# Performance work log

Hardware: AMD Instinct MI355X
Metric: run time of the kernel (lower is better)

The kernel has to match this reference:

```python
import jax, jax.numpy as jnp
import numpy as np

K = 3          # stencil half-width
SIGMA = 0.05   # shock proximity length scale
DX = 0.02      # spatial step
HID = 64       # flux net hidden dim
IN_FEAT = (2 * K + 1) * 3 + 1  # 22


def setup_inputs() -> dict:
    key = jax.random.key(0)
    ks = jax.random.split(key, 10)
    B, nt, nx = 16, 64, 1024
    grid_input = jax.random.uniform(ks[0], (B, 1, nt, nx), jnp.float32)
    dt = jax.random.uniform(ks[1], (B,), jnp.float32) * 0.01  # CFL-like dt
    s = lambda k, sh: jax.random.normal(k, sh, jnp.float32) * 0.1
    return {
        "grid_input": grid_input,
        "dt": dt,
        "W0": s(ks[2], (HID, IN_FEAT)), "b0": s(ks[3], (HID,)),
        "W1": s(ks[4], (HID, HID)),     "b1": s(ks[5], (HID,)),
        "W2": s(ks[6], (HID, HID)),     "b2": s(ks[7], (HID,)),
        "W3": s(ks[8], (1, HID)),       "b3": s(ks[9], (1,)),
    }


def reference(grid_input, dt, W0, b0, W1, b1, W2, b2, W3, b3):
    B, _, nt, nx = grid_input.shape
    k, dx, S = K, DX, 2 * K + 1
    dtype = grid_input.dtype

    # static gather indices for the stencil unfold (into the padded array)
    idx = jnp.arange(nx)[:, None] + jnp.arange(S)[None, :]  # (nx, S)
    # static distance matrix cell-center vs interface (computed once, reused every step)
    cell_centers = (jnp.arange(nx, dtype=dtype) + 0.5) * dx          # (nx,)
    interface_pos = jnp.arange(1, nx, dtype=dtype) * dx              # (nx-1,)
    dist = jnp.abs(cell_centers[:, None] - interface_pos[None, :])   # (nx, nx-1)

    dt3 = dt[:, None, None]  # (B,1,1)

    def unfold(x):  # (B,1,nx) -> (B,S,nx) replicate-padded sliding windows
        p = jnp.pad(x[:, 0, :], ((0, 0), (k, k)), mode="edge")  # (B, nx+2k)
        return jnp.transpose(p[:, idx], (0, 2, 1))              # (B,S,nx)

    def shock_proximity(state):  # (B,1,nx) -> (B,1,nx), detached
        st = jax.lax.stop_gradient(state)
        rL, rR = st[:, 0, :-1], st[:, 0, 1:]
        char_L = 1.0 - 2.0 * rL           # f'(rho) for LWR flux rho(1-rho)
        char_R = 1.0 - 2.0 * rR
        s_rh = 1.0 - rL - rR              # Rankine-Hugoniot shock speed
        is_shock = (char_L > s_rh) & (s_rh > char_R)      # (B, nx-1)
        masked = jnp.where(is_shock[:, None, :], dist[None], jnp.asarray(1e6, dtype))
        min_dist = masked.min(axis=2)                     # (B, nx)
        any_shock = jnp.any(is_shock, axis=1, keepdims=True).astype(dtype)
        return (jnp.exp(-min_dist / SIGMA) * any_shock)[:, None, :]

    gelu = lambda h: jax.nn.gelu(h, approximate=False)

    def flux_net(f):  # (B, IN_FEAT, nx) -> (B, 1, nx); dropout inactive (eval)
        h = jnp.einsum("oc,bcn->bon", W0, f) + b0[None, :, None]
        h = jnp.einsum("oc,bcn->bon", W1, gelu(h)) + b1[None, :, None]
        h = jnp.einsum("oc,bcn->bon", W2, gelu(h)) + b2[None, :, None]
        return jnp.einsum("oc,bcn->bon", W3, gelu(h)) + b3[None, :, None]

    def step(state, _):
        stencil_vals = unfold(state)                      # (B,S,nx)
        char_speeds = 1.0 - 2.0 * stencil_vals            # flux.derivative
        prox = shock_proximity(state)                     # (B,1,nx)
        stencil_prox = unfold(prox)                       # (B,S,nx)
        dt_channel = jnp.broadcast_to(dt3, (B, 1, nx))
        feats = jnp.concatenate([stencil_vals, char_speeds, stencil_prox, dt_channel], axis=1)
        update = flux_net(feats)                          # (B,1,nx)
        new_state = jnp.clip(state + dt3 / dx * update, 0.0, 1.0)
        return new_state, new_state

    state0 = grid_input[:, :, 0, :]                       # (B,1,nx)
    _, ys = jax.lax.scan(step, state0, None, length=nt - 1)  # (nt-1,B,1,nx)
    out = jnp.concatenate([state0[:, :, None, :], jnp.transpose(ys, (1, 2, 0, 3))], axis=2)
    return out  # (B,1,nt,nx)
```

## Files before the change

kernel.cpp:

```cpp
#include <hip/hip_runtime.h>

#define NX 1024
#define NT 64
#define NBATCH 16
#define BPB 64
#define NBLK (NBATCH * BPB)
#define DXC 0.02f
#define INV_SIG 20.0f
#define BIGF 1.0e6f

typedef __attribute__((ext_vector_type(8))) short bf16x8;
typedef __attribute__((ext_vector_type(4))) float f32x4;
typedef unsigned long long u64t;

__device__ __forceinline__ unsigned short f2bf(float x) {
    unsigned u = __builtin_bit_cast(unsigned, x);
    u += 0x7FFFu + ((u >> 16) & 1u);
    return (unsigned short)(u >> 16);
}
__device__ __forceinline__ float bf2f(unsigned short h) {
    return __builtin_bit_cast(float, (unsigned)h << 16);
}
__device__ __forceinline__ unsigned cvt_pk_bf16(float lo, float hi) {
    unsigned r;
    asm("v_cvt_pk_bf16_f32 %0, %1, %2" : "=v"(r) : "v"(lo), "v"(hi));
    return r;
}
__device__ __forceinline__ float hw_exp2(float v) {
    float e;
    asm("v_exp_f32 %0, %1" : "=v"(e) : "v"(v));
    return e;
}

__device__ __forceinline__ float fast_gelu(float x) {
    float x2 = x * x;
    float v  = x * fmaf(0.1029456f, x2, 2.3022654f);
    float rc = __builtin_amdgcn_rcpf(hw_exp2(v) + 1.0f);
    return x - x * rc;
}

__device__ __forceinline__ u64t sys_load_u64(const u64t* p) {
    return __hip_atomic_load(p, __ATOMIC_RELAXED, __HIP_MEMORY_SCOPE_SYSTEM);
}
__device__ __forceinline__ void sys_store_u64(u64t* p, u64t v) {
    __hip_atomic_store(p, v, __ATOMIC_RELAXED, __HIP_MEMORY_SCOPE_SYSTEM);
}

__device__ __forceinline__ int swz(int row, int k) {
    return (row << 6) + ((((k >> 3) ^ row) & 7) << 3) + (k & 7);
}

__global__ void __launch_bounds__(256, 4) nfv_kernel(
    const float* __restrict__ grid, const float* __restrict__ dtp,
    const float* __restrict__ W0, const float* __restrict__ b0,
    const float* __restrict__ W1, const float* __restrict__ b1,
    const float* __restrict__ W2, const float* __restrict__ b2,
    const float* __restrict__ W3, const float* __restrict__ b3,
    float* __restrict__ outp, u64t* __restrict__ halo)
{
    __shared__ float st_s[80];
    __shared__ __align__(16) unsigned short feat_s[16 * 64];
    __shared__ __align__(16) unsigned short actA[16 * 64];
    __shared__ __align__(16) unsigned short actB[16 * 64];
    __shared__ __align__(16) float part_s[16 * 20];

    const int tid  = threadIdx.x;
    const int lane = tid & 63;
    const int wid  = tid >> 6;
    const int bid  = blockIdx.x;
    const int b    = bid >> 6;
    const int bb   = bid & 63;
    const int c0   = bb * 16;
    const float dtv = dtp[b];
    const float r   = dtv / DXC;
    const float b3v = b3[0];

    const float* grow = grid + (size_t)b * (NT * NX);
    float*       orow = outp + (size_t)b * (NT * NX);

    const int l15 = lane & 15;
    const int kb0 = lane >> 4;
    const int col = wid * 16 + l15;
    const int row0 = (lane >> 4) << 2;
    const int arow = l15;

    bf16x8 w0f, w1fa, w1fb, w2fa, w2fb;
    {
        const int k0 = kb0 * 8;
        #pragma unroll
        for (int i = 0; i < 8; ++i) {
            int k = k0 + i;
            float wv;
            if (k < 7)       wv = W0[col * 22 + k] - 2.0f * W0[col * 22 + 7 + k];
            else if (k < 14) wv = W0[col * 22 + (k - 7)] - 2.0f * W0[col * 22 + k];
            else if (k < 22) wv = W0[col * 22 + k];
            else             wv = 0.0f;
            w0f[i]  = (short)f2bf(wv);
            w1fa[i] = (short)f2bf(W1[col * 64 + k0 + i]);
            w1fb[i] = (short)f2bf(W1[col * 64 + k0 + 32 + i]);
            w2fa[i] = (short)f2bf(W2[col * 64 + k0 + i]);
            w2fb[i] = (short)f2bf(W2[col * 64 + k0 + 32 + i]);
        }
    }
    float bias0 = b0[col];
    #pragma unroll
    for (int k = 7; k < 14; ++k) bias0 += W0[col * 22 + k];
    const float bias1 = b1[col], bias2 = b2[col], w3c = W3[col];

    const int aoffA = (arow << 6) + (((kb0    ) ^ arow) * 8 & 56);
    const int aoffB = (arow << 6) + ((((kb0+4) ^ arow) & 7) << 3);
    const bf16x8* const prF  = (const bf16x8*)(const void*)&feat_s[aoffA];
    const bf16x8* const prA0 = (const bf16x8*)(const void*)&actA[aoffA];
    const bf16x8* const prA1 = (const bf16x8*)(const void*)&actA[aoffB];
    const bf16x8* const prB0 = (const bf16x8*)(const void*)&actB[aoffA];
    const bf16x8* const prB1 = (const bf16x8*)(const void*)&actB[aoffB];
    unsigned short* const pwA0 = &actA[swz(row0    , col)];
    unsigned short* const pwA1 = &actA[swz(row0 + 1, col)];
    unsigned short* const pwA2 = &actA[swz(row0 + 2, col)];
    unsigned short* const pwA3 = &actA[swz(row0 + 3, col)];
    unsigned short* const pwB0 = &actB[swz(row0    , col)];
    unsigned short* const pwB1 = &actB[swz(row0 + 1, col)];
    unsigned short* const pwB2 = &actB[swz(row0 + 2, col)];
    unsigned short* const pwB3 = &actB[swz(row0 + 3, col)];
    const int poff = row0 * 20 + (wid << 2) + (l15 >> 2);
    const bool pwrite = ((l15 & 3) == 0);

    const int fslot = wid * 2 + (lane >> 5);
    const int frow  = lane & 15;
    const bool fact = (fslot < 7) && ((lane & 31) < 16);
    int fc = frow + 29 + fslot;
    if (bb == 0       && fc < 32) fc = 32;
    if (bb == BPB - 1 && fc > 47) fc = 47;
    const int foff0 = swz(frow, fslot);
    const int foff1 = swz(frow, 7 + fslot);
    const int foff2 = swz(frow, 14 + fslot);

    int hg = (lane < 32) ? (c0 - 32 + lane) : (c0 - 16 + lane);
    hg = hg < 0 ? 0 : (hg > NX - 1 ? NX - 1 : hg);
    const u64t* const hbase = &halo[(size_t)(b * BPB + (hg >> 4)) * 64 + (hg & 15)];
    const int hdst = (lane < 32) ? lane : lane + 16;

    const f32x4* const pru = (const f32x4*)(const void*)&part_s[l15 * 20];
    u64t* const hpub = &halo[(size_t)bid * 64 + l15];
    float* const ocell = orow + c0 + l15;

    ((unsigned*)feat_s)[tid]       = 0;
    ((unsigned*)feat_s)[tid + 256] = 0;
    if (tid < 16) {
        orow[c0 + tid] = grow[c0 + tid];
        feat_s[swz(tid, 21)] = f2bf(dtv);
    }
    if (tid < 80) {
        int ga = c0 - 32 + tid;
        ga = ga < 0 ? 0 : (ga > NX - 1 ? NX - 1 : ga);
        st_s[tid] = grow[ga];
    }

    for (int t = 1; t < NT; ++t) {
        if (wid == 0 && t >= 2) {
            const unsigned need = (unsigned)(t - 1);
            const u64t* src = hbase + (size_t)(((t - 1) & 3) * 16);
            u64t u;
            do { u = sys_load_u64(src); } while ((unsigned)(u >> 32) < need);
            st_s[hdst] = __builtin_bit_cast(float, (unsigned)u);
        }
        __syncthreads();

        {
            bool q0 = st_s[lane + 1] > st_s[lane];
            bool q1 = (lane < 15) && (st_s[65 + lane] > st_s[64 + lane]);
            u64t m0 = __ballot(q0);
            u64t m1 = __ballot(q1);
            if (fact) {
                const int c = fc;
                float dL = BIGF, dR = BIGF;
                u64t sello = m0 & (((u64t)1 << c) - 1);
                if (sello) dL = (float)(c - (63 - __builtin_clzll(sello))) - 0.5f;
                u64t r0 = m0 >> c;
                if (r0)      dR = (float)__builtin_ctzll(r0) + 0.5f;
                else if (m1) dR = (float)(64 - c + __builtin_ctzll(m1)) + 0.5f;
                float d = fminf(dL, dR);
                float prox = hw_exp2(d * -0.5770780f);

                float sv = st_s[c];
                unsigned short shi = f2bf(sv);
                unsigned short slo = f2bf(sv - bf2f(shi));
                feat_s[foff0] = shi;
                feat_s[foff1] = slo;
                feat_s[foff2] = f2bf(prox);
            }
        }
        __syncthreads();

        {
            f32x4 c4 = {0.0f, 0.0f, 0.0f, 0.0f};
            c4 = __builtin_amdgcn_mfma_f32_16x16x32_bf16(*prF, w0f, c4, 0, 0, 0);
            unsigned u01 = cvt_pk_bf16(fast_gelu(c4[0] + bias0), fast_gelu(c4[1] + bias0));
            unsigned u23 = cvt_pk_bf16(fast_gelu(c4[2] + bias0), fast_gelu(c4[3] + bias0));
            *pwA0 = (unsigned short)u01;
            *pwA1 = (unsigned short)(u01 >> 16);
            *pwA2 = (unsigned short)u23;
            *pwA3 = (unsigned short)(u23 >> 16);
        }
        __syncthreads();

        {
            f32x4 c4 = {0.0f, 0.0f, 0.0f, 0.0f};
            c4 = __builtin_amdgcn_mfma_f32_16x16x32_bf16(*prA0, w1fa, c4, 0, 0, 0);
            c4 = __builtin_amdgcn_mfma_f32_16x16x32_bf16(*prA1, w1fb, c4, 0, 0, 0);
            unsigned u01 = cvt_pk_bf16(fast_gelu(c4[0] + bias1), fast_gelu(c4[1] + bias1));
            unsigned u23 = cvt_pk_bf16(fast_gelu(c4[2] + bias1), fast_gelu(c4[3] + bias1));
            *pwB0 = (unsigned short)u01;
            *pwB1 = (unsigned short)(u01 >> 16);
            *pwB2 = (unsigned short)u23;
            *pwB3 = (unsigned short)(u23 >> 16);
        }
        __syncthreads();

        {
            f32x4 c4 = {0.0f, 0.0f, 0.0f, 0.0f};
            c4 = __builtin_amdgcn_mfma_f32_16x16x32_bf16(*prB0, w2fa, c4, 0, 0, 0);
            c4 = __builtin_amdgcn_mfma_f32_16x16x32_bf16(*prB1, w2fb, c4, 0, 0, 0);
            #pragma unroll
            for (int j = 0; j < 4; ++j) {
                float p = w3c * fast_gelu(c4[j] + bias2);
                p += __shfl_xor(p, 1);
                p += __shfl_xor(p, 2);
                if (pwrite) part_s[poff + j * 20] = p;
            }
        }
        __syncthreads();

        if (wid == 0 && lane < 16) {
            f32x4 s4 = pru[0] + pru[1] + pru[2] + pru[3];
            float sum = s4[0] + s4[1] + s4[2] + s4[3];
            float ns = st_s[32 + l15] + r * (sum + b3v);
            ns = fminf(1.0f, fmaxf(0.0f, ns));
            if (t < NT - 1) {
                u64t u = ((u64t)(unsigned)t << 32) |
                         (u64t)(unsigned)__builtin_bit_cast(unsigned, ns);
                sys_store_u64(hpub + (size_t)((t & 3) * 16), u);
            }
            ocell[(size_t)t * NX] = ns;
            st_s[32 + l15] = ns;
        }
    }
}

extern "C" void kernel_launch(void* const* d_in, const int* in_sizes, int n_in,
                              void* d_out, int out_size, void* d_ws, size_t ws_size,
                              hipStream_t stream) {
    const float* grid = (const float*)d_in[0];
    const float* dtp  = (const float*)d_in[1];
    const float* W0   = (const float*)d_in[2];
    const float* b0   = (const float*)d_in[3];
    const float* W1   = (const float*)d_in[4];
    const float* b1   = (const float*)d_in[5];
    const float* W2   = (const float*)d_in[6];
    const float* b2   = (const float*)d_in[7];
    const float* W3   = (const float*)d_in[8];
    const float* b3   = (const float*)d_in[9];
    float* outp = (float*)d_out;

    u64t* halo = (u64t*)d_ws;

    hipMemsetAsync(d_ws, 0, (size_t)NBLK * 64 * sizeof(u64t), stream);

    void* args[] = {(void*)&grid, (void*)&dtp, (void*)&W0, (void*)&b0,
                    (void*)&W1, (void*)&b1, (void*)&W2, (void*)&b2,
                    (void*)&W3, (void*)&b3, (void*)&outp, (void*)&halo};

    int maxb = 0;
    hipError_t qe = hipOccupancyMaxActiveBlocksPerMultiprocessor(
        &maxb, (const void*)nfv_kernel, 256, 0);
    if (qe == hipSuccess && maxb >= 4) {
        hipLaunchCooperativeKernel((const void*)nfv_kernel,
                                   dim3(NBLK), dim3(256), args, 0, stream);
    } else {
        hipLaunchKernelGGL(nfv_kernel, dim3(NBLK), dim3(256), 0, stream,
                           grid, dtp, W0, b0, W1, b1, W2, b2, W3, b3,
                           outp, halo);
    }
}
```

Before: 188.4 us.

## Collapse each block to a single wavefront and replace barriers with wave fences

Each 256-thread block becomes one 64-lane wavefront that computes all four 16-column output tiles of every MLP layer itself. This lets the per-layer __syncthreads barriers become lgkmcnt waits, and the cross-wave partial-sum LDS reduction becomes in-register shuffles. State values are kept in registers, and GELU is written in a paired-float form. The cost is four times the MFMA and GELU work per wave and more register pressure, while the same 1024 blocks must still stay co-resident for the halo spin-waits.

```diff
diff --git a/kernel.cpp b/kernel.cpp
--- a/kernel.cpp
+++ b/kernel.cpp
@@ -6,11 +6,11 @@
 #define BPB 64
 #define NBLK (NBATCH * BPB)
 #define DXC 0.02f
-#define INV_SIG 20.0f
 #define BIGF 1.0e6f
 
 typedef __attribute__((ext_vector_type(8))) short bf16x8;
 typedef __attribute__((ext_vector_type(4))) float f32x4;
+typedef __attribute__((ext_vector_type(2))) float f32x2;
 typedef unsigned long long u64t;
 
 __device__ __forceinline__ unsigned short f2bf(float x) {
@@ -32,10 +32,12 @@
     return e;
 }
 
-__device__ __forceinline__ float fast_gelu(float x) {
-    float x2 = x * x;
-    float v  = x * fmaf(0.1029456f, x2, 2.3022654f);
-    float rc = __builtin_amdgcn_rcpf(hw_exp2(v) + 1.0f);
+__device__ __forceinline__ f32x2 pk_gelu(f32x2 x) {
+    f32x2 x2 = x * x;
+    f32x2 v  = x * (x2 * 0.1029456f + 2.3022654f);
+    f32x2 rc;
+    rc.x = __builtin_amdgcn_rcpf(hw_exp2(v.x) + 1.0f);
+    rc.y = __builtin_amdgcn_rcpf(hw_exp2(v.y) + 1.0f);
     return x - x * rc;
 }
 
@@ -50,7 +52,12 @@
     return (row << 6) + ((((k >> 3) ^ row) & 7) << 3) + (k & 7);
 }
 
-__global__ void __launch_bounds__(256, 4) nfv_kernel(
+__device__ __forceinline__ void wave_fence() {
+    asm volatile("s_waitcnt lgkmcnt(0)" ::: "memory");
+    __builtin_amdgcn_sched_barrier(0);
+}
+
+__global__ void __launch_bounds__(64, 1) nfv_kernel(
     const float* __restrict__ grid, const float* __restrict__ dtp,
     const float* __restrict__ W0, const float* __restrict__ b0,
     const float* __restrict__ W1, const float* __restrict__ b1,
@@ -62,11 +69,8 @@
     __shared__ __align__(16) unsigned short feat_s[16 * 64];
     __shared__ __align__(16) unsigned short actA[16 * 64];
     __shared__ __align__(16) unsigned short actB[16 * 64];
-    __shared__ __align__(16) float part_s[16 * 20];
-
-    const int tid  = threadIdx.x;
-    const int lane = tid & 63;
-    const int wid  = tid >> 6;
+
+    const int lane = threadIdx.x;
     const int bid  = blockIdx.x;
     const int b    = bid >> 6;
     const int bb   = bid & 63;
@@ -80,99 +84,109 @@
 
     const int l15 = lane & 15;
     const int kb0 = lane >> 4;
-    const int col = wid * 16 + l15;
-    const int row0 = (lane >> 4) << 2;
-    const int arow = l15;
-
-    bf16x8 w0f, w1fa, w1fb, w2fa, w2fb;
-    {
-        const int k0 = kb0 * 8;
+    const int row0 = kb0 << 2;
+    const int k0  = kb0 * 8;
+
+    bf16x8 w0f[4], w1fa[4], w1fb[4], w2fa[4], w2fb[4];
+    float bias0[4], bias1[4], bias2[4], w3c[4];
+    #pragma unroll
+    for (int tt = 0; tt < 4; ++tt) {
+        const int colt = tt * 16 + l15;
         #pragma unroll
         for (int i = 0; i < 8; ++i) {
             int k = k0 + i;
             float wv;
-            if (k < 7)       wv = W0[col * 22 + k] - 2.0f * W0[col * 22 + 7 + k];
-            else if (k < 14) wv = W0[col * 22 + (k - 7)] - 2.0f * W0[col * 22 + k];
-            else if (k < 22) wv = W0[col * 22 + k];
+            if (k < 7)       wv = W0[colt * 22 + k] - 2.0f * W0[colt * 22 + 7 + k];
+            else if (k < 14) wv = W0[colt * 22 + (k - 7)] - 2.0f * W0[colt * 22 + k];
+            else if (k < 22) wv = W0[colt * 22 + k];
             else             wv = 0.0f;
-            w0f[i]  = (short)f2bf(wv);
-            w1fa[i] = (short)f2bf(W1[col * 64 + k0 + i]);
-            w1fb[i] = (short)f2bf(W1[col * 64 + k0 + 32 + i]);
-            w2fa[i] = (short)f2bf(W2[col * 64 + k0 + i]);
-            w2fb[i] = (short)f2bf(W2[col * 64 + k0 + 32 + i]);
-        }
-    }
-    float bias0 = b0[col];
-    #pragma unroll
-    for (int k = 7; k < 14; ++k) bias0 += W0[col * 22 + k];
-    const float bias1 = b1[col], bias2 = b2[col], w3c = W3[col];
-
-    const int aoffA = (arow << 6) + (((kb0    ) ^ arow) * 8 & 56);
-    const int aoffB = (arow << 6) + ((((kb0+4) ^ arow) & 7) << 3);
+            w0f[tt][i]  = (short)f2bf(wv);
+            w1fa[tt][i] = (short)f2bf(W1[colt * 64 + k0 + i]);
+            w1fb[tt][i] = (short)f2bf(W1[colt * 64 + k0 + 32 + i]);
+            w2fa[tt][i] = (short)f2bf(W2[colt * 64 + k0 + i]);
+            w2fb[tt][i] = (short)f2bf(W2[colt * 64 + k0 + 32 + i]);
+        }
+        float bb0 = b0[colt];
+        #pragma unroll
+        for (int k = 7; k < 14; ++k) bb0 += W0[colt * 22 + k];
+        bias0[tt] = bb0;
+        bias1[tt] = b1[colt];
+        bias2[tt] = b2[colt];
+        w3c[tt]   = W3[colt];
+    }
+
+    const int aoffA = (l15 << 6) + ((((kb0    ) ^ l15) & 7) << 3);
+    const int aoffB = (l15 << 6) + ((((kb0 + 4) ^ l15) & 7) << 3);
     const bf16x8* const prF  = (const bf16x8*)(const void*)&feat_s[aoffA];
     const bf16x8* const prA0 = (const bf16x8*)(const void*)&actA[aoffA];
     const bf16x8* const prA1 = (const bf16x8*)(const void*)&actA[aoffB];
     const bf16x8* const prB0 = (const bf16x8*)(const void*)&actB[aoffA];
     const bf16x8* const prB1 = (const bf16x8*)(const void*)&actB[aoffB];
-    unsigned short* const pwA0 = &actA[swz(row0    , col)];
-    unsigned short* const pwA1 = &actA[swz(row0 + 1, col)];
-    unsigned short* const pwA2 = &actA[swz(row0 + 2, col)];
-    unsigned short* const pwA3 = &actA[swz(row0 + 3, col)];
-    unsigned short* const pwB0 = &actB[swz(row0    , col)];
-    unsigned short* const pwB1 = &actB[swz(row0 + 1, col)];
-    unsigned short* const pwB2 = &actB[swz(row0 + 2, col)];
-    unsigned short* const pwB3 = &actB[swz(row0 + 3, col)];
-    const int poff = row0 * 20 + (wid << 2) + (l15 >> 2);
-    const bool pwrite = ((l15 & 3) == 0);
-
-    const int fslot = wid * 2 + (lane >> 5);
-    const int frow  = lane & 15;
-    const bool fact = (fslot < 7) && ((lane & 31) < 16);
-    int fc = frow + 29 + fslot;
-    if (bb == 0       && fc < 32) fc = 32;
-    if (bb == BPB - 1 && fc > 47) fc = 47;
-    const int foff0 = swz(frow, fslot);
-    const int foff1 = swz(frow, 7 + fslot);
-    const int foff2 = swz(frow, 14 + fslot);
+
+    int soff[16];
+    #pragma unroll
+    for (int tt = 0; tt < 4; ++tt)
+        #pragma unroll
+        for (int j = 0; j < 4; ++j)
+            soff[tt * 4 + j] = swz(row0 + j, tt * 16 + l15);
+
+    int fc0 = l15 + 29 + kb0;
+    int fc1 = l15 + 29 + kb0 + 4;
+    if (bb == 0)   { if (fc0 < 32) fc0 = 32; if (fc1 < 32) fc1 = 32; }
+    if (bb == BPB - 1) { if (fc0 > 47) fc0 = 47; if (fc1 > 47) fc1 = 47; }
+    const bool fact1 = (kb0 < 3);
+    const int f0a = swz(l15, kb0),     f0b = swz(l15, 7 + kb0),  f0c = swz(l15, 14 + kb0);
+    const int f1a = swz(l15, kb0 + 4), f1b = swz(l15, 11 + kb0), f1c = swz(l15, 18 + kb0);
 
     int hg = (lane < 32) ? (c0 - 32 + lane) : (c0 - 16 + lane);
     hg = hg < 0 ? 0 : (hg > NX - 1 ? NX - 1 : hg);
     const u64t* const hbase = &halo[(size_t)(b * BPB + (hg >> 4)) * 64 + (hg & 15)];
     const int hdst = (lane < 32) ? lane : lane + 16;
 
-    const f32x4* const pru = (const f32x4*)(const void*)&part_s[l15 * 20];
-    u64t* const hpub = &halo[(size_t)bid * 64 + l15];
-    float* const ocell = orow + c0 + l15;
-
-    ((unsigned*)feat_s)[tid]       = 0;
-    ((unsigned*)feat_s)[tid + 256] = 0;
-    if (tid < 16) {
-        orow[c0 + tid] = grow[c0 + tid];
-        feat_s[swz(tid, 21)] = f2bf(dtv);
-    }
-    if (tid < 80) {
-        int ga = c0 - 32 + tid;
+    const bool upd = (l15 == 0);
+    u64t* const hpub = &halo[(size_t)bid * 64 + row0];
+    float st_reg[4];
+    #pragma unroll
+    for (int j = 0; j < 4; ++j) st_reg[j] = grow[c0 + row0 + j];
+
+    #pragma unroll
+    for (int i = 0; i < 8; ++i) ((unsigned*)feat_s)[lane + 64 * i] = 0;
+    if (lane < 16) {
+        orow[c0 + lane] = grow[c0 + lane];
+        feat_s[swz(lane, 21)] = f2bf(dtv);
+    }
+    {
+        int ga = c0 - 32 + lane;
         ga = ga < 0 ? 0 : (ga > NX - 1 ? NX - 1 : ga);
-        st_s[tid] = grow[ga];
-    }
+        st_s[lane] = grow[ga];
+        if (lane < 16) {
+            int gb = c0 + 32 + lane;
+            gb = gb > NX - 1 ? NX - 1 : gb;
+            st_s[64 + lane] = grow[gb];
+        }
+    }
+    wave_fence();
 
     for (int t = 1; t < NT; ++t) {
-        if (wid == 0 && t >= 2) {
+        if (t >= 2) {
             const unsigned need = (unsigned)(t - 1);
             const u64t* src = hbase + (size_t)(((t - 1) & 3) * 16);
             u64t u;
             do { u = sys_load_u64(src); } while ((unsigned)(u >> 32) < need);
             st_s[hdst] = __builtin_bit_cast(float, (unsigned)u);
-        }
-        __syncthreads();
+            wave_fence();
+        }
 
         {
             bool q0 = st_s[lane + 1] > st_s[lane];
             bool q1 = (lane < 15) && (st_s[65 + lane] > st_s[64 + lane]);
             u64t m0 = __ballot(q0);
             u64t m1 = __ballot(q1);
-            if (fact) {
-                const int c = fc;
+
+            #pragma unroll
+            for (int pass = 0; pass < 2; ++pass) {
+                if (pass == 1 && !fact1) break;
+                const int c = pass ? fc1 : fc0;
                 float dL = BIGF, dR = BIGF;
                 u64t sello = m0 & (((u64t)1 << c) - 1);
                 if (sello) dL = (float)(c - (63 - __builtin_clzll(sello))) - 0.5f;
@@ -181,69 +195,109 @@
                 else if (m1) dR = (float)(64 - c + __builtin_ctzll(m1)) + 0.5f;
                 float d = fminf(dL, dR);
                 float prox = hw_exp2(d * -0.5770780f);
-
                 float sv = st_s[c];
                 unsigned short shi = f2bf(sv);
                 unsigned short slo = f2bf(sv - bf2f(shi));
-                feat_s[foff0] = shi;
-                feat_s[foff1] = slo;
-                feat_s[foff2] = f2bf(prox);
-            }
-        }
-        __syncthreads();
+                feat_s[pass ? f1a : f0a] = shi;
+                feat_s[pass ? f1b : f0b] = slo;
+                feat_s[pass ? f1c : f0c] = f2bf(prox);
+            }
+        }
+        wave_fence();
 
         {
-            f32x4 c4 = {0.0f, 0.0f, 0.0f, 0.0f};
-            c4 = __builtin_amdgcn_mfma_f32_16x16x32_bf16(*prF, w0f, c4, 0, 0, 0);
-            unsigned u01 = cvt_pk_bf16(fast_gelu(c4[0] + bias0), fast_gelu(c4[1] + bias0));
-            unsigned u23 = cvt_pk_bf16(fast_gelu(c4[2] + bias0), fast_gelu(c4[3] + bias0));
-            *pwA0 = (unsigned short)u01;
-            *pwA1 = (unsigned short)(u01 >> 16);
-            *pwA2 = (unsigned short)u23;
-            *pwA3 = (unsigned short)(u23 >> 16);
-        }
-        __syncthreads();
+            bf16x8 aF = *prF;
+            f32x4 c4[4];
+            #pragma unroll
+            for (int tt = 0; tt < 4; ++tt) {
+                c4[tt] = (f32x4){bias0[tt], bias0[tt], bias0[tt], bias0[tt]};
+                c4[tt] = __builtin_amdgcn_mfma_f32_16x16x32_bf16(aF, w0f[tt], c4[tt], 0, 0, 0);
+            }
+            #pragma unroll
+            for (int tt = 0; tt < 4; ++tt) {
+                f32x2 g01 = pk_gelu((f32x2){c4[tt][0], c4[tt][1]});
+                f32x2 g23 = pk_gelu((f32x2){c4[tt][2], c4[tt][3]});
+                unsigned u01 = cvt_pk_bf16(g01.x, g01.y);
+                unsigned u23 = cvt_pk_bf16(g23.x, g23.y);
+                actA[soff[tt * 4 + 0]] = (unsigned short)u01;
+                actA[soff[tt * 4 + 1]] = (unsigned short)(u01 >> 16);
+                actA[soff[tt * 4 + 2]] = (unsigned short)u23;
+                actA[soff[tt * 4 + 3]] = (unsigned short)(u23 >> 16);
+            }
+        }
+        wave_fence();
 
         {
-            f32x4 c4 = {0.0f, 0.0f, 0.0f, 0.0f};
-            c4 = __builtin_amdgcn_mfma_f32_16x16x32_bf16(*prA0, w1fa, c4, 0, 0, 0);
-            c4 = __builtin_amdgcn_mfma_f32_16x16x32_bf16(*prA1, w1fb, c4, 0, 0, 0);
-            unsigned u01 = cvt_pk_bf16(fast_gelu(c4[0] + bias1), fast_gelu(c4[1] + bias1));
-            unsigned u23 = cvt_pk_bf16(fast_gelu(c4[2] + bias1), fast_gelu(c4[3] + bias1));
-            *pwB0 = (unsigned short)u01;
-            *pwB1 = (unsigned short)(u01 >> 16);
-            *pwB2 = (unsigned short)u23;
-            *pwB3 = (unsigned short)(u23 >> 16);
-        }
-        __syncthreads();
-
+            bf16x8 a0 = *prA0, a1 = *prA1;
+            f32x4 c4[4];
+            #pragma unroll
+            for (int tt = 0; tt < 4; ++tt) {
+                c4[tt] = (f32x4){bias1[tt], bias1[tt], bias1[tt], bias1[tt]};
+                c4[tt] = __builtin_amdgcn_mfma_f32_16x16x32_bf16(a0, w1fa[tt], c4[tt], 0, 0, 0);
+                c4[tt] = __builtin_amdgcn_mfma_f32_16x16x32_bf16(a1, w1fb[tt], c4[tt], 0, 0, 0);
+            }
+            #pragma unroll
+            for (int tt = 0; tt < 4; ++tt) {
+                f32x2 g01 = pk_gelu((f32x2){c4[tt][0], c4[tt][1]});
+                f32x2 g23 = pk_gelu((f32x2){c4[tt][2], c4[tt][3]});
+                unsigned u01 = cvt_pk_bf16(g01.x, g01.y);
+                unsigned u23 = cvt_pk_bf16(g23.x, g23.y);
+                actB[soff[tt * 4 + 0]] = (unsigned short)u01;
+                actB[soff[tt * 4 + 1]] = (unsigned short)(u01 >> 16);
+                actB[soff[tt * 4 + 2]] = (unsigned short)u23;
+                actB[soff[tt * 4 + 3]] = (unsigned short)(u23 >> 16);
+            }
+        }
+        wave_fence();
+
+        float sum0, sum1, sum2, sum3;
         {
-            f32x4 c4 = {0.0f, 0.0f, 0.0f, 0.0f};
-            c4 = __builtin_amdgcn_mfma_f32_16x16x32_bf16(*prB0, w2fa, c4, 0, 0, 0);
-            c4 = __builtin_amdgcn_mfma_f32_16x16x32_bf16(*prB1, w2fb, c4, 0, 0, 0);
+            bf16x8 a0 = *prB0, a1 = *prB1;
+            f32x4 c4[4];
+            #pragma unroll
+            for (int tt = 0; tt < 4; ++tt) {
+                c4[tt] = (f32x4){bias2[tt], bias2[tt], bias2[tt], bias2[tt]};
+                c4[tt] = __builtin_amdgcn_mfma_f32_16x16x32_bf16(a0, w2fa[tt], c4[tt], 0, 0, 0);
+                c4[tt] = __builtin_amdgcn_mfma_f32_16x16x32_bf16(a1, w2fb[tt], c4[tt], 0, 0, 0);
+            }
+            float p0 = 0.0f, p1 = 0.0f, p2 = 0.0f, p3 = 0.0f;
+            #pragma unroll
+            for (int tt = 0; tt < 4; ++tt) {
+                f32x2 g01 = pk_gelu((f32x2){c4[tt][0], c4[tt][1]});
+                f32x2 g23 = pk_gelu((f32x2){c4[tt][2], c4[tt][3]});
+                p0 += w3c[tt] * g01.x;
+                p1 += w3c[tt] * g01.y;
+                p2 += w3c[tt] * g23.x;
+                p3 += w3c[tt] * g23.y;
+            }
+            p0 += __shfl_xor(p0, 1); p0 += __shfl_xor(p0, 2);
+            p0 += __shfl_xor(p0, 4); p0 += __shfl_xor(p0, 8);
+            p1 += __shfl_xor(p1, 1); p1 += __shfl_xor(p1, 2);
+            p1 += __shfl_xor(p1, 4); p1 += __shfl_xor(p1, 8);
+            p2 += __shfl_xor(p2, 1); p2 += __shfl_xor(p2, 2);
+            p2 += __shfl_xor(p2, 4); p2 += __shfl_xor(p2, 8);
+            p3 += __shfl_xor(p3, 1); p3 += __shfl_xor(p3, 2);
+            p3 += __shfl_xor(p3, 4); p3 += __shfl_xor(p3, 8);
+            sum0 = p0; sum1 = p1; sum2 = p2; sum3 = p3;
+        }
+
+        if (upd) {
+            float sums[4] = {sum0, sum1, sum2, sum3};
             #pragma unroll
             for (int j = 0; j < 4; ++j) {
-                float p = w3c * fast_gelu(c4[j] + bias2);
-                p += __shfl_xor(p, 1);
-                p += __shfl_xor(p, 2);
-                if (pwrite) part_s[poff + j * 20] = p;
-            }
-        }
-        __syncthreads();
-
-        if (wid == 0 && lane < 16) {
-            f32x4 s4 = pru[0] + pru[1] + pru[2] + pru[3];
-            float sum = s4[0] + s4[1] + s4[2] + s4[3];
-            float ns = st_s[32 + l15] + r * (sum + b3v);
-            ns = fminf(1.0f, fmaxf(0.0f, ns));
-            if (t < NT - 1) {
-                u64t u = ((u64t)(unsigned)t << 32) |
-                         (u64t)(unsigned)__builtin_bit_cast(unsigned, ns);
-                sys_store_u64(hpub + (size_t)((t & 3) * 16), u);
-            }
-            ocell[(size_t)t * NX] = ns;
-            st_s[32 + l15] = ns;
-        }
+                float ns = st_reg[j] + r * (sums[j] + b3v);
+                ns = fminf(1.0f, fmaxf(0.0f, ns));
+                st_reg[j] = ns;
+                if (t < NT - 1) {
+                    u64t u = ((u64t)(unsigned)t << 32) |
+                             (u64t)(unsigned)__builtin_bit_cast(unsigned, ns);
+                    sys_store_u64(hpub + (size_t)((t & 3) * 16) + j, u);
+                }
+                orow[(size_t)t * NX + c0 + row0 + j] = ns;
+                st_s[32 + row0 + j] = ns;
+            }
+        }
+        wave_fence();
     }
 }
 
@@ -272,12 +326,12 @@
 
     int maxb = 0;
     hipError_t qe = hipOccupancyMaxActiveBlocksPerMultiprocessor(
-        &maxb, (const void*)nfv_kernel, 256, 0);
+        &maxb, (const void*)nfv_kernel, 64, 0);
     if (qe == hipSuccess && maxb >= 4) {
         hipLaunchCooperativeKernel((const void*)nfv_kernel,
-                                   dim3(NBLK), dim3(256), args, 0, stream);
+                                   dim3(NBLK), dim3(64), args, 0, stream);
     } else {
-        hipLaunchKernelGGL(nfv_kernel, dim3(NBLK), dim3(256), 0, stream,
+        hipLaunchKernelGGL(nfv_kernel, dim3(NBLK), dim3(64), 0, stream,
                            grid, dtp, W0, b0, W1, b1, W2, b2, W3, b3,
                            outp, halo);
     }
```

Result: slower. 200.1 us (+6.2%).
